# Kernel tuning notes

Measured on AMD Instinct MI355X. Metric: run time of the kernel, lower is better.

Reference implementation:

```python
import jax, jax.numpy as jnp
import numpy as np

B, S, DK = 32, 2048, 64

def setup_inputs() -> dict:
    key = jax.random.key(0)
    kq, kk, kv = jax.random.split(key, 3)
    Q = jax.random.normal(kq, (B, S, DK), dtype=jnp.float32)
    K = jax.random.normal(kk, (B, S, DK), dtype=jnp.float32)
    V = jax.random.normal(kv, (B, S, DK), dtype=jnp.float32)
    return {"Q": Q, "K": K, "V": V}

def reference(Q, K, V):
    # attn_scores = Q K^T / sqrt(d_k); full [B,S,S] probs materialized (naive, non-flash)
    d_k = Q.shape[-1]
    scores = jnp.einsum('bqd,bkd->bqk', Q, K) / jnp.sqrt(jnp.asarray(d_k, Q.dtype))
    probs = jax.nn.softmax(scores, axis=-1)
    return jnp.einsum('bqk,bkd->bqd', probs, V)
```

## Files before the change

### kernel.cpp

```cpp
#include <hip/hip_runtime.h>

#define BATCH 32
#define SEQ   2048
#define DKK   64

constexpr int QT = 128;
constexpr int KT = 64;
constexpr int NW = 4;
constexpr int WQ = 32;

typedef __attribute__((ext_vector_type(8))) short bf16x8;
typedef __attribute__((ext_vector_type(4))) float f32x4;
typedef __attribute__((ext_vector_type(4))) short short4v;

__device__ __forceinline__ short f2bf(float f) {
    union { float f; unsigned u; } c; c.f = f;
    unsigned r = c.u + 0x7fffu + ((c.u >> 16) & 1u);
    return (short)(r >> 16);
}

__device__ __forceinline__ float fast_exp2(float x) {
#if __has_builtin(__builtin_amdgcn_exp2f)
    return __builtin_amdgcn_exp2f(x);
#else
    return exp2f(x);
#endif
}

__global__ __launch_bounds__(256, 2) void attn_fwd(
        const float* __restrict__ Q, const float* __restrict__ K,
        const float* __restrict__ V, float* __restrict__ O) {
    __shared__ short Kb[KT][DKK + 8];
    __shared__ short Vt[DKK][KT + 8];
    __shared__ short Pb[NW][WQ][KT + 8];

    const int tid  = threadIdx.x;
    const int w    = tid >> 6;
    const int lane = tid & 63;
    const int quad = lane >> 4;
    const int l15  = lane & 15;
    const int b    = blockIdx.y;
    const int q0   = blockIdx.x * QT + w * WQ;

    const float qscale = 0.125f * 1.44269504088896340736f;
    bf16x8 qfrag[2][2];
    #pragma unroll
    for (int mt = 0; mt < 2; ++mt) {
      #pragma unroll
      for (int ks = 0; ks < 2; ++ks) {
        const float* qp = Q + ((size_t)b * SEQ + q0 + 16*mt + l15) * DKK + 32*ks + quad*8;
        float4 a = *(const float4*)qp;
        float4 c = *(const float4*)(qp + 4);
        bf16x8 f;
        f[0]=f2bf(a.x*qscale); f[1]=f2bf(a.y*qscale); f[2]=f2bf(a.z*qscale); f[3]=f2bf(a.w*qscale);
        f[4]=f2bf(c.x*qscale); f[5]=f2bf(c.y*qscale); f[6]=f2bf(c.z*qscale); f[7]=f2bf(c.w*qscale);
        qfrag[mt][ks] = f;
      }
    }

    f32x4 o[2][4] = {};
    float lsum[2][4] = {};

    const float* Kbase = K + (size_t)b * SEQ * DKK;
    const float* Vbase = V + (size_t)b * SEQ * DKK;

    for (int kb = 0; kb < SEQ; kb += KT) {
        __syncthreads();
        {
            const float* Kg = Kbase + (size_t)kb * DKK;
            #pragma unroll
            for (int i = 0; i < 4; ++i) {
                int f   = tid + 256*i;
                int row = f >> 4;
                int c4  = (f & 15) << 2;
                float4 kv = *(const float4*)(Kg + row*DKK + c4);
                short4v kk;
                kk[0]=f2bf(kv.x); kk[1]=f2bf(kv.y); kk[2]=f2bf(kv.z); kk[3]=f2bf(kv.w);
                *(short4v*)&Kb[row][c4] = kk;
            }
            const float* Vg = Vbase + (size_t)(kb + w*16) * DKK + lane;
            #pragma unroll
            for (int c = 0; c < 4; ++c) {
                short4v t;
                #pragma unroll
                for (int i = 0; i < 4; ++i) t[i] = f2bf(Vg[(4*c + i) * DKK]);
                *(short4v*)&Vt[lane][w*16 + 4*c] = t;
            }
        }
        __syncthreads();

        bf16x8 kfrag[4][2];
        #pragma unroll
        for (int nt = 0; nt < 4; ++nt)
          #pragma unroll
          for (int ks = 0; ks < 2; ++ks)
            kfrag[nt][ks] = *(const bf16x8*)&Kb[16*nt + l15][32*ks + quad*8];

        f32x4 sc[2][4];
        #pragma unroll
        for (int mt = 0; mt < 2; ++mt)
          #pragma unroll
          for (int nt = 0; nt < 4; ++nt) {
            f32x4 acc = {};
            acc = __builtin_amdgcn_mfma_f32_16x16x32_bf16(qfrag[mt][0], kfrag[nt][0], acc, 0, 0, 0);
            acc = __builtin_amdgcn_mfma_f32_16x16x32_bf16(qfrag[mt][1], kfrag[nt][1], acc, 0, 0, 0);
            sc[mt][nt] = acc;
          }

        #pragma unroll
        for (int mt = 0; mt < 2; ++mt)
          #pragma unroll
          for (int nt = 0; nt < 4; ++nt)
            #pragma unroll
            for (int j = 0; j < 4; ++j) {
              float p = fast_exp2(sc[mt][nt][j]);
              lsum[mt][j] += p;
              Pb[w][16*mt + 4*quad + j][16*nt + l15] = f2bf(p);
            }

        #pragma unroll
        for (int ks = 0; ks < 2; ++ks) {
          bf16x8 pa0 = *(const bf16x8*)&Pb[w][l15     ][32*ks + quad*8];
          bf16x8 pa1 = *(const bf16x8*)&Pb[w][16 + l15][32*ks + quad*8];
          #pragma unroll
          for (int nt = 0; nt < 4; ++nt) {
            bf16x8 vf = *(const bf16x8*)&Vt[16*nt + l15][32*ks + quad*8];
            o[0][nt] = __builtin_amdgcn_mfma_f32_16x16x32_bf16(pa0, vf, o[0][nt], 0, 0, 0);
            o[1][nt] = __builtin_amdgcn_mfma_f32_16x16x32_bf16(pa1, vf, o[1][nt], 0, 0, 0);
          }
        }
    }

    #pragma unroll
    for (int mt = 0; mt < 2; ++mt)
      #pragma unroll
      for (int j = 0; j < 4; ++j) {
        float s = lsum[mt][j];
        s += __shfl_xor(s, 1);
        s += __shfl_xor(s, 2);
        s += __shfl_xor(s, 4);
        s += __shfl_xor(s, 8);
        lsum[mt][j] = 1.0f / s;
      }

    #pragma unroll
    for (int mt = 0; mt < 2; ++mt)
      #pragma unroll
      for (int j = 0; j < 4; ++j) {
        float inv = lsum[mt][j];
        float* op = O + ((size_t)b * SEQ + q0 + 16*mt + 4*quad + j) * DKK + l15;
        #pragma unroll
        for (int nt = 0; nt < 4; ++nt)
          op[16*nt] = o[mt][nt][j] * inv;
      }
}

extern "C" void kernel_launch(void* const* d_in, const int* in_sizes, int n_in,
                              void* d_out, int out_size, void* d_ws, size_t ws_size,
                              hipStream_t stream) {
    const float* Q = (const float*)d_in[0];
    const float* K = (const float*)d_in[1];
    const float* V = (const float*)d_in[2];
    float* O = (float*)d_out;
    dim3 grid(SEQ / QT, BATCH);
    attn_fwd<<<grid, dim3(256), 0, stream>>>(Q, K, V, O);
}
```

Before: 153.2 us.

## Remap blocks for L2 locality, raise occupancy, and restructure V transpose loads

Block indices are remapped so that consecutive workgroups are spread across batches in a pattern meant to fit the per-XCD L2 sharing of K/V tiles. Launch bounds go from 2 to 4 blocks per CU to raise occupancy. The V transpose load is reindexed so each quad reads different rows and lanes write different Vt rows, which changes the global coalescing and LDS bank pattern. K fragments are now loaded per n-tile inside the QK loop, which lowers live registers. The risks are register spills under the tighter launch bound and a remap that hardcodes the grid shape.

```diff
diff --git a/kernel.cpp b/kernel.cpp
--- a/kernel.cpp
+++ b/kernel.cpp
@@ -27,25 +27,29 @@
 #endif
 }
 
-__global__ __launch_bounds__(256, 2) void attn_fwd(
+__global__ __launch_bounds__(256, 4) void attn_fwd(
         const float* __restrict__ Q, const float* __restrict__ K,
         const float* __restrict__ V, float* __restrict__ O) {
-    __shared__ short Kb[KT][DKK + 8];
-    __shared__ short Vt[DKK][KT + 8];
-    __shared__ short Pb[NW][WQ][KT + 8];
+    __shared__ short Kb[KT][72];
+    __shared__ short Vt[DKK][72];
+    __shared__ short Pb[NW][WQ][72];
 
     const int tid  = threadIdx.x;
     const int w    = tid >> 6;
     const int lane = tid & 63;
     const int quad = lane >> 4;
     const int l15  = lane & 15;
-    const int b    = blockIdx.y;
-    const int q0   = blockIdx.x * QT + w * WQ;
+    const int kq   = quad;
+
+    const int l  = blockIdx.x + gridDim.x * blockIdx.y;
+    const int b  = (l & 7) * 4 + (l >> 7);
+    const int qt = (l >> 3) & 15;
+    const int q0 = qt * QT + w * WQ;
 
     const float qscale = 0.125f * 1.44269504088896340736f;
     bf16x8 qfrag[2][2];
     #pragma unroll
-    for (int mt = 0; mt < 2; ++mt) {
+    for (int mt = 0; mt < 2; ++mt)
       #pragma unroll
       for (int ks = 0; ks < 2; ++ks) {
         const float* qp = Q + ((size_t)b * SEQ + q0 + 16*mt + l15) * DKK + 32*ks + quad*8;
@@ -56,13 +60,12 @@
         f[4]=f2bf(c.x*qscale); f[5]=f2bf(c.y*qscale); f[6]=f2bf(c.z*qscale); f[7]=f2bf(c.w*qscale);
         qfrag[mt][ks] = f;
       }
-    }
 
     f32x4 o[2][4] = {};
     float lsum[2][4] = {};
 
     const float* Kbase = K + (size_t)b * SEQ * DKK;
-    const float* Vbase = V + (size_t)b * SEQ * DKK;
+    const float* Vg0 = V + (size_t)b * SEQ * DKK + (size_t)(w*16 + 4*kq) * DKK + l15;
 
     for (int kb = 0; kb < SEQ; kb += KT) {
         __syncthreads();
@@ -78,34 +81,30 @@
                 kk[0]=f2bf(kv.x); kk[1]=f2bf(kv.y); kk[2]=f2bf(kv.z); kk[3]=f2bf(kv.w);
                 *(short4v*)&Kb[row][c4] = kk;
             }
-            const float* Vg = Vbase + (size_t)(kb + w*16) * DKK + lane;
+            const float* Vrow = Vg0 + (size_t)kb * DKK;
             #pragma unroll
             for (int c = 0; c < 4; ++c) {
                 short4v t;
                 #pragma unroll
-                for (int i = 0; i < 4; ++i) t[i] = f2bf(Vg[(4*c + i) * DKK]);
-                *(short4v*)&Vt[lane][w*16 + 4*c] = t;
+                for (int i = 0; i < 4; ++i) t[i] = f2bf(Vrow[i*DKK + 16*c]);
+                *(short4v*)&Vt[16*c + l15][w*16 + 4*kq] = t;
             }
         }
         __syncthreads();
 
-        bf16x8 kfrag[4][2];
-        #pragma unroll
-        for (int nt = 0; nt < 4; ++nt)
-          #pragma unroll
-          for (int ks = 0; ks < 2; ++ks)
-            kfrag[nt][ks] = *(const bf16x8*)&Kb[16*nt + l15][32*ks + quad*8];
-
         f32x4 sc[2][4];
         #pragma unroll
-        for (int mt = 0; mt < 2; ++mt)
-          #pragma unroll
-          for (int nt = 0; nt < 4; ++nt) {
-            f32x4 acc = {};
-            acc = __builtin_amdgcn_mfma_f32_16x16x32_bf16(qfrag[mt][0], kfrag[nt][0], acc, 0, 0, 0);
-            acc = __builtin_amdgcn_mfma_f32_16x16x32_bf16(qfrag[mt][1], kfrag[nt][1], acc, 0, 0, 0);
-            sc[mt][nt] = acc;
-          }
+        for (int nt = 0; nt < 4; ++nt) {
+            bf16x8 kf0 = *(const bf16x8*)&Kb[16*nt + l15][quad*8];
+            bf16x8 kf1 = *(const bf16x8*)&Kb[16*nt + l15][32 + quad*8];
+            #pragma unroll
+            for (int mt = 0; mt < 2; ++mt) {
+                f32x4 acc = {};
+                acc = __builtin_amdgcn_mfma_f32_16x16x32_bf16(qfrag[mt][0], kf0, acc, 0, 0, 0);
+                acc = __builtin_amdgcn_mfma_f32_16x16x32_bf16(qfrag[mt][1], kf1, acc, 0, 0, 0);
+                sc[mt][nt] = acc;
+            }
+        }
 
         #pragma unroll
         for (int mt = 0; mt < 2; ++mt)
@@ -113,21 +112,21 @@
           for (int nt = 0; nt < 4; ++nt)
             #pragma unroll
             for (int j = 0; j < 4; ++j) {
-              float p = fast_exp2(sc[mt][nt][j]);
-              lsum[mt][j] += p;
-              Pb[w][16*mt + 4*quad + j][16*nt + l15] = f2bf(p);
+                float p = fast_exp2(sc[mt][nt][j]);
+                lsum[mt][j] += p;
+                Pb[w][16*mt + 4*quad + j][16*nt + l15] = f2bf(p);
             }
 
         #pragma unroll
         for (int ks = 0; ks < 2; ++ks) {
-          bf16x8 pa0 = *(const bf16x8*)&Pb[w][l15     ][32*ks + quad*8];
-          bf16x8 pa1 = *(const bf16x8*)&Pb[w][16 + l15][32*ks + quad*8];
-          #pragma unroll
-          for (int nt = 0; nt < 4; ++nt) {
-            bf16x8 vf = *(const bf16x8*)&Vt[16*nt + l15][32*ks + quad*8];
-            o[0][nt] = __builtin_amdgcn_mfma_f32_16x16x32_bf16(pa0, vf, o[0][nt], 0, 0, 0);
-            o[1][nt] = __builtin_amdgcn_mfma_f32_16x16x32_bf16(pa1, vf, o[1][nt], 0, 0, 0);
-          }
+            bf16x8 pa0 = *(const bf16x8*)&Pb[w][l15     ][32*ks + quad*8];
+            bf16x8 pa1 = *(const bf16x8*)&Pb[w][16 + l15][32*ks + quad*8];
+            #pragma unroll
+            for (int nt = 0; nt < 4; ++nt) {
+                bf16x8 vf = *(const bf16x8*)&Vt[16*nt + l15][32*ks + quad*8];
+                o[0][nt] = __builtin_amdgcn_mfma_f32_16x16x32_bf16(pa0, vf, o[0][nt], 0, 0, 0);
+                o[1][nt] = __builtin_amdgcn_mfma_f32_16x16x32_bf16(pa1, vf, o[1][nt], 0, 0, 0);
+            }
         }
     }
 
@@ -151,7 +150,7 @@
         float* op = O + ((size_t)b * SEQ + q0 + 16*mt + 4*quad + j) * DKK + l15;
         #pragma unroll
         for (int nt = 0; nt < 4; ++nt)
-          op[16*nt] = o[mt][nt][j] * inv;
+            op[16*nt] = o[mt][nt][j] * inv;
       }
 }
 
```

Measured after the change: 185.4 us. 1.21x slower.
